# Optimization experiments

Hardware: AMD Instinct MI355X
Metric: run time of the kernel (lower is better)

The kernel has to match this reference:

```python
import jax, jax.numpy as jnp
import numpy as np

D_MODEL = 512
N_HEADS = 8
D_K = D_MODEL // N_HEADS


def setup_inputs() -> dict:
    key = jax.random.key(0)
    ks = jax.random.split(key, 7)
    s = 1.0 / np.sqrt(D_MODEL)
    return {
        "x": jax.random.normal(ks[0], (2, 4096, D_MODEL), dtype=jnp.float32),
        "W_q": jax.random.normal(ks[1], (D_MODEL, D_MODEL), dtype=jnp.float32) * s,
        "W_k": jax.random.normal(ks[2], (D_MODEL, D_MODEL), dtype=jnp.float32) * s,
        "W_v": jax.random.normal(ks[3], (D_MODEL, D_MODEL), dtype=jnp.float32) * s,
        "b_v": jax.random.normal(ks[4], (D_MODEL,), dtype=jnp.float32) * s,
        "W_o": jax.random.normal(ks[5], (D_MODEL, D_MODEL), dtype=jnp.float32) * s,
        "b_o": jax.random.normal(ks[6], (D_MODEL,), dtype=jnp.float32) * s,
    }


def _split_heads(t):
    # [N, S, d_model] -> [N, H, S, d_k]
    N, S, _ = t.shape
    return t.reshape(N, S, N_HEADS, D_K).transpose(0, 2, 1, 3)


def reference(x, W_q, W_k, W_v, b_v, W_o, b_o):
    N, S, _ = x.shape
    # nn.Linear computes x @ W.T (+ b)
    Q = _split_heads(x @ W_q.T)
    K = _split_heads(x @ W_k.T)
    V = _split_heads(x @ W_v.T + b_v)
    scale = jnp.sqrt(jnp.asarray(D_K, x.dtype))
    scores = jnp.einsum('nhqd,nhkd->nhqk', Q, K) / scale  # [N,H,S,S]
    causal = jnp.tril(jnp.ones((S, S), dtype=bool))
    scores = jnp.where(causal, scores, -jnp.inf)
    attn = jax.nn.softmax(scores, axis=-1)
    out = jnp.einsum('nhqk,nhkd->nhqd', attn, V)  # [N,H,S,d_k]
    out = out.transpose(0, 2, 1, 3).reshape(N, S, D_MODEL)
    return out @ W_o.T + b_o
```

## Files before the change

### kernel.cpp

```cpp
#include <hip/hip_runtime.h>
#include <hip/hip_bf16.h>

#define NB 2
#define SEQ 4096
#define DM 512
#define NH 8
#define DKH 64
#define MTOT (NB*SEQ)

typedef __attribute__((ext_vector_type(4))) float f32x4;
typedef __attribute__((ext_vector_type(16))) float f32x16;
typedef __attribute__((ext_vector_type(8))) short bf16x8;
typedef __attribute__((ext_vector_type(2))) unsigned uint2v;

__device__ inline unsigned short f2bf(float f) {
    union { float f; unsigned int u; } v; v.f = f;
    unsigned int r = v.u + 0x7FFFu + ((v.u >> 16) & 1u);
    return (unsigned short)(r >> 16);
}

#define QSCALE 0.18033688011112042f

__global__ void cast_kernel(const float* __restrict__ x, const float* __restrict__ wq,
                            const float* __restrict__ wk, const float* __restrict__ wv,
                            const float* __restrict__ wo, unsigned short* __restrict__ dst) {
    const int NX = MTOT*DM;
    const int NW = DM*DM;
    int i4 = blockIdx.x * blockDim.x + threadIdx.x;
    long e = (long)i4 * 4;
    if (e >= NX + 4L*NW) return;
    const float* src; long off;
    if (e < NX)           { src = x;  off = e; }
    else if (e < NX+NW)   { src = wq; off = e - NX; }
    else if (e < NX+2*NW) { src = wk; off = e - NX - NW; }
    else if (e < NX+3*NW) { src = wv; off = e - NX - 2*NW; }
    else                  { src = wo; off = e - NX - 3*NW; }
    float4 v = *reinterpret_cast<const float4*>(src + off);
    ushort4 o;
    o.x = f2bf(v.x); o.y = f2bf(v.y); o.z = f2bf(v.z); o.w = f2bf(v.w);
    *reinterpret_cast<ushort4*>(dst + e) = o;
}

template<int MODE>
__global__ __launch_bounds__(256, 2) void gemm_bt(
    const unsigned short* __restrict__ A,
    const unsigned short* __restrict__ B,
    const float* __restrict__ bias,
    unsigned short* __restrict__ Qh, unsigned short* __restrict__ Kh,
    unsigned short* __restrict__ Vt,
    float* __restrict__ Cout)
{
    const int K = 512;
    __shared__ __align__(16) unsigned short As[128*64];
    __shared__ __align__(16) unsigned short Bs[128*64];
    int tid = threadIdx.x;
    int wid = tid >> 6, lane = tid & 63;
    int wr = wid >> 1, wc = wid & 1;
    int brow = blockIdx.x * 128;
    int bcol = blockIdx.y * 128;
    int l15 = lane & 15, l4 = lane >> 4;

    f32x4 acc[4][4] = {};

    for (int kt = 0; kt < K/64; ++kt) {
        __syncthreads();
        #pragma unroll
        for (int i = 0; i < 4; ++i) {
            int rbase = i*32 + wid*8;
            int row = rbase + (lane >> 3);
            int csrc = (lane & 7) ^ (row & 7);
            const unsigned short* asrc = A + (long)(brow+row)*K + kt*64 + csrc*8;
            __builtin_amdgcn_global_load_lds(
                (const __attribute__((address_space(1))) unsigned int*)asrc,
                (__attribute__((address_space(3))) unsigned int*)&As[rbase*64], 16, 0, 0);
            const unsigned short* bsrc = B + (long)(bcol+row)*K + kt*64 + csrc*8;
            __builtin_amdgcn_global_load_lds(
                (const __attribute__((address_space(1))) unsigned int*)bsrc,
                (__attribute__((address_space(3))) unsigned int*)&Bs[rbase*64], 16, 0, 0);
        }
        __syncthreads();
        #pragma unroll
        for (int kk = 0; kk < 2; ++kk) {
            bf16x8 af[4], bfr[4];
            #pragma unroll
            for (int mi = 0; mi < 4; ++mi) {
                int row = wr*64 + mi*16 + l15;
                int colb = (kk*32 + l4*8) * 2;
                af[mi] = *reinterpret_cast<const bf16x8*>(
                    reinterpret_cast<const char*>(As) + row*128 + (colb ^ ((row&7)<<4)));
            }
            #pragma unroll
            for (int ni = 0; ni < 4; ++ni) {
                int row = wc*64 + ni*16 + l15;
                int colb = (kk*32 + l4*8) * 2;
                bfr[ni] = *reinterpret_cast<const bf16x8*>(
                    reinterpret_cast<const char*>(Bs) + row*128 + (colb ^ ((row&7)<<4)));
            }
            #pragma unroll
            for (int mi = 0; mi < 4; ++mi)
                #pragma unroll
                for (int ni = 0; ni < 4; ++ni)
                    acc[mi][ni] = __builtin_amdgcn_mfma_f32_16x16x32_bf16(af[mi], bfr[ni], acc[mi][ni], 0, 0, 0);
        }
    }

    #pragma unroll
    for (int mi = 0; mi < 4; ++mi) {
        #pragma unroll
        for (int ni = 0; ni < 4; ++ni) {
            #pragma unroll
            for (int r = 0; r < 4; ++r) {
                int row = brow + wr*64 + mi*16 + l4*4 + r;
                int col = bcol + wc*64 + ni*16 + l15;
                float v = acc[mi][ni][r];
                if (MODE == 0) {
                    int which = col >> 9;
                    int cw = col & 511;
                    int h = cw >> 6, d = cw & 63;
                    int b = row >> 12, s = row & 4095;
                    int bh = b*NH + h;
                    if (which == 0) {
                        Qh[((long)(bh*SEQ + s))*DKH + d] = f2bf(v * QSCALE);
                    } else if (which == 1) {
                        Kh[((long)(bh*SEQ + s))*DKH + d] = f2bf(v);
                    } else {
                        Vt[((long)(bh*DKH + d))*SEQ + s] = f2bf(v + bias[cw]);
                    }
                } else {
                    Cout[(long)row*DM + col] = v + bias[col];
                }
            }
        }
    }
}

__global__ __launch_bounds__(256, 2) void attn_kernel(
    const unsigned short* __restrict__ Qh,
    const unsigned short* __restrict__ Kh,
    const unsigned short* __restrict__ Vt,
    unsigned short* __restrict__ Obf)
{
    __shared__ __align__(16) unsigned short Klds[2][8448];
    __shared__ __align__(16) unsigned short Vlds[2][8448];
    const int tid = threadIdx.x;
    const int wid = tid >> 6, lane = tid & 63;
    const int l31 = lane & 31;
    const int hi  = lane >> 5;
    const int bh  = blockIdx.x;
    const int ty  = blockIdx.y;
    const int tile = ty < 16 ? 31 - ty : ty - 16;

    const unsigned short* Qbase = Qh + (long)bh*SEQ*DKH;
    const unsigned short* Kbase = Kh + (long)bh*SEQ*DKH;
    const unsigned short* Vbase = Vt + (long)bh*DKH*SEQ;

    const int q0w = tile*128 + wid*32;
    const int q   = q0w + l31;
    const int nt  = tile + 1;
    const int swz   = (l31 & 7) << 4;
    const int lbase = (l31 >> 3)*1056 + (l31 & 7)*128;

    bf16x8 qf[4];
    #pragma unroll
    for (int kk = 0; kk < 4; ++kk)
        qf[kk] = *reinterpret_cast<const bf16x8*>(Qbase + (long)q*DKH + kk*16 + hi*8);

    auto STAGE = [&](int b, int key0) {
        #pragma unroll
        for (int ii = 0; ii < 4; ++ii) {
            const int row = wid*32 + ii*8 + (lane >> 3);
            const int ck = (lane & 7) ^ (row & 7);
            const unsigned short* ksrc = Kbase + (long)(key0 + row)*DKH + ck*8;
            __builtin_amdgcn_global_load_lds(
                (const __attribute__((address_space(1))) unsigned int*)ksrc,
                (__attribute__((address_space(3))) unsigned int*)&Klds[b][(wid*4 + ii)*528], 16, 0, 0);
        }
        #pragma unroll
        for (int jj = 0; jj < 2; ++jj) {
            #pragma unroll
            for (int ii = 0; ii < 2; ++ii) {
                const int row = wid*16 + ii*8 + (lane >> 3);
                const int ck = (lane & 7) ^ (row & 7);
                const unsigned short* vsrc = Vbase + (long)row*SEQ + key0 + jj*64 + ck*8;
                __builtin_amdgcn_global_load_lds(
                    (const __attribute__((address_space(1))) unsigned int*)vsrc,
                    (__attribute__((address_space(3))) unsigned int*)&Vlds[b][(jj*8 + wid*2 + ii)*528], 16, 0, 0);
            }
        }
    };

    float m = -1e30f, lsum = 0.f;
    f32x16 od0 = {}, od1 = {};

    STAGE(0, 0);
    __syncthreads();
    int cur = 0;

    for (int kb = 0; kb < nt; ++kb) {
        if (kb + 1 < nt) STAGE(cur ^ 1, (kb + 1) << 7);
        const char* kl = reinterpret_cast<const char*>(Klds[cur]);
        const char* vl = reinterpret_cast<const char*>(Vlds[cur]);
        const int key0 = kb << 7;

        bf16x8 kfr[4][4];
        #pragma unroll
        for (int kk = 0; kk < 4; ++kk) {
            const int co = (kk*32 + hi*16) ^ swz;
            #pragma unroll
            for (int c = 0; c < 4; ++c)
                kfr[kk][c] = *reinterpret_cast<const bf16x8*>(kl + lbase + c*4224 + co);
        }
        f32x16 s0 = {}, s1 = {}, s2 = {}, s3 = {};
        __builtin_amdgcn_s_setprio(1);
        #pragma unroll
        for (int kk = 0; kk < 4; ++kk) {
            s0 = __builtin_amdgcn_mfma_f32_32x32x16_bf16(kfr[kk][0], qf[kk], s0, 0, 0, 0);
            s1 = __builtin_amdgcn_mfma_f32_32x32x16_bf16(kfr[kk][1], qf[kk], s1, 0, 0, 0);
            s2 = __builtin_amdgcn_mfma_f32_32x32x16_bf16(kfr[kk][2], qf[kk], s2, 0, 0, 0);
            s3 = __builtin_amdgcn_mfma_f32_32x32x16_bf16(kfr[kk][3], qf[kk], s3, 0, 0, 0);
        }
        __builtin_amdgcn_s_setprio(0);

        if (key0 + 127 > q0w) {
            #pragma unroll
            for (int r = 0; r < 16; ++r) {
                const int ko = (r&3) + 8*(r>>2) + 4*hi;
                if (key0 + ko > q)      s0[r] = -1e30f;
                if (key0 + 32 + ko > q) s1[r] = -1e30f;
                if (key0 + 64 + ko > q) s2[r] = -1e30f;
                if (key0 + 96 + ko > q) s3[r] = -1e30f;
            }
        }

        float pmax = s0[0];
        #pragma unroll
        for (int r = 1; r < 16; ++r) pmax = fmaxf(pmax, s0[r]);
        #pragma unroll
        for (int r = 0; r < 16; ++r) pmax = fmaxf(pmax, fmaxf(s1[r], fmaxf(s2[r], s3[r])));
        {
            uint2v pr = __builtin_amdgcn_permlane32_swap(__float_as_uint(pmax), __float_as_uint(pmax), false, false);
            pmax = fmaxf(__uint_as_float(pr[0]), __uint_as_float(pr[1]));
        }

        if (__any(pmax > m + 6.0f)) {
            const float mn = fmaxf(m, pmax);
            const float alpha = __builtin_amdgcn_exp2f(m - mn);
            m = mn;
            lsum *= alpha;
            #pragma unroll
            for (int r = 0; r < 16; ++r) { od0[r] *= alpha; od1[r] *= alpha; }
        }

        float rsc0 = 0.f, rsc1 = 0.f, rsc2 = 0.f, rsc3 = 0.f;
#define EXP_CHUNK(SV, RS) do {                                                     \
        _Pragma("unroll")                                                          \
        for (int r = 0; r < 16; ++r) {                                             \
            SV[r] = __builtin_amdgcn_exp2f(SV[r] - m);                             \
            RS += SV[r];                                                           \
        } } while (0)

#define PV_STEP(SV, VBASE, KS, B0) do {                                            \
        unsigned c0, c1, c2, c3;                                                   \
        float t0 = SV[B0+0], t1 = SV[B0+1], t2 = SV[B0+2], t3 = SV[B0+3];          \
        float t4 = SV[B0+4], t5 = SV[B0+5], t6 = SV[B0+6], t7 = SV[B0+7];          \
        asm("v_cvt_pk_bf16_f32 %0, %1, %2" : "=v"(c0) : "v"(t0), "v"(t1));         \
        asm("v_cvt_pk_bf16_f32 %0, %1, %2" : "=v"(c1) : "v"(t2), "v"(t3));         \
        asm("v_cvt_pk_bf16_f32 %0, %1, %2" : "=v"(c2) : "v"(t4), "v"(t5));         \
        asm("v_cvt_pk_bf16_f32 %0, %1, %2" : "=v"(c3) : "v"(t6), "v"(t7));         \
        uint2v sw0 = __builtin_amdgcn_permlane32_swap(c0, c2, false, false);       \
        uint2v sw1 = __builtin_amdgcn_permlane32_swap(c1, c3, false, false);       \
        union { unsigned u[4]; bf16x8 v; } pu;                                     \
        pu.u[0] = sw0[0]; pu.u[1] = sw1[0]; pu.u[2] = sw0[1]; pu.u[3] = sw1[1];    \
        bf16x8 vf0 = *reinterpret_cast<const bf16x8*>(VBASE + lbase +        (((KS)*32 + hi*16) ^ swz)); \
        od0 = __builtin_amdgcn_mfma_f32_32x32x16_bf16(vf0, pu.v, od0, 0, 0, 0);    \
        bf16x8 vf1 = *reinterpret_cast<const bf16x8*>(VBASE + lbase + 4224 + (((KS)*32 + hi*16) ^ swz)); \
        od1 = __builtin_amdgcn_mfma_f32_32x32x16_bf16(vf1, pu.v, od1, 0, 0, 0);    \
    } while (0)

        const char* vl0 = vl;
        const char* vl1 = vl + 8448;
        EXP_CHUNK(s0, rsc0);
        PV_STEP(s0, vl0, 0, 0);
        PV_STEP(s0, vl0, 1, 8);
        EXP_CHUNK(s1, rsc1);
        PV_STEP(s1, vl0, 2, 0);
        PV_STEP(s1, vl0, 3, 8);
        EXP_CHUNK(s2, rsc2);
        PV_STEP(s2, vl1, 0, 0);
        PV_STEP(s2, vl1, 1, 8);
        EXP_CHUNK(s3, rsc3);
        PV_STEP(s3, vl1, 2, 0);
        PV_STEP(s3, vl1, 3, 8);
#undef PV_STEP
#undef EXP_CHUNK
        lsum += (rsc0 + rsc1) + (rsc2 + rsc3);

        __syncthreads();
        cur ^= 1;
    }

    {
        uint2v pr = __builtin_amdgcn_permlane32_swap(__float_as_uint(lsum), __float_as_uint(lsum), false, false);
        lsum = __uint_as_float(pr[0]) + __uint_as_float(pr[1]);
    }
    const float rls = 1.0f / lsum;
    const long obase = (long)((bh >> 3)*SEQ + q)*DM + (bh & 7)*DKH;
    #pragma unroll
    for (int rr = 0; rr < 4; ++rr) {
        ushort4 w0, w1;
        w0.x = f2bf(od0[rr*4+0]*rls); w0.y = f2bf(od0[rr*4+1]*rls);
        w0.z = f2bf(od0[rr*4+2]*rls); w0.w = f2bf(od0[rr*4+3]*rls);
        *reinterpret_cast<ushort4*>(Obf + obase + rr*8 + hi*4) = w0;
        w1.x = f2bf(od1[rr*4+0]*rls); w1.y = f2bf(od1[rr*4+1]*rls);
        w1.z = f2bf(od1[rr*4+2]*rls); w1.w = f2bf(od1[rr*4+3]*rls);
        *reinterpret_cast<ushort4*>(Obf + obase + 32 + rr*8 + hi*4) = w1;
    }
}

extern "C" void kernel_launch(void* const* d_in, const int* in_sizes, int n_in,
                              void* d_out, int out_size, void* d_ws, size_t ws_size,
                              hipStream_t stream) {
    const float* x  = (const float*)d_in[0];
    const float* wq = (const float*)d_in[1];
    const float* wk = (const float*)d_in[2];
    const float* wv = (const float*)d_in[3];
    const float* bv = (const float*)d_in[4];
    const float* wo = (const float*)d_in[5];
    const float* bo = (const float*)d_in[6];
    float* out = (float*)d_out;

    unsigned short* ws = (unsigned short*)d_ws;
    unsigned short* Xbf  = ws;
    unsigned short* Wqkv = Xbf  + 4194304;
    unsigned short* Wob  = Wqkv + 786432;
    unsigned short* Qh   = Wob  + 262144;
    unsigned short* Kh   = Qh   + 4194304;
    unsigned short* Vt   = Kh   + 4194304;
    unsigned short* Obf  = Vt   + 4194304;

    cast_kernel<<<5120, 256, 0, stream>>>(x, wq, wk, wv, wo, Xbf);

    dim3 g1(64, 12);
    gemm_bt<0><<<g1, 256, 0, stream>>>(Xbf, Wqkv, bv, Qh, Kh, Vt, nullptr);

    dim3 g2(16, 32);
    attn_kernel<<<g2, 256, 0, stream>>>(Qh, Kh, Vt, Obf);

    dim3 g3(64, 4);
    gemm_bt<1><<<g3, 256, 0, stream>>>(Obf, Wob, bo, nullptr, nullptr, nullptr, out);
}
```

Measured before the change: 121.3 us.

## Pair complementary 64-query causal tiles per 2-wave attention block

The attention kernel drops from 4 waves per block to 2 waves of 128 threads. Each block now processes two 64-query tiles in sequence, tile 63-ty and tile ty, so every block does about the same causal work. The LDS K/V buffers lose their padded row stride and rely only on the XOR swizzle, and launch bounds allow more registers per thread. In exchange, each staged 128-key K/V tile now serves only 64 queries, which doubles K/V load traffic. Each CU also holds fewer resident waves, and diagonal 128-key blocks waste some masked work for 64-query tiles.

```diff
diff --git a/kernel.cpp b/kernel.cpp
--- a/kernel.cpp
+++ b/kernel.cpp
@@ -134,186 +134,194 @@
     }
 }
 
-__global__ __launch_bounds__(256, 2) void attn_kernel(
+__global__ __launch_bounds__(128, 1) void attn_kernel(
     const unsigned short* __restrict__ Qh,
     const unsigned short* __restrict__ Kh,
     const unsigned short* __restrict__ Vt,
     unsigned short* __restrict__ Obf)
 {
-    __shared__ __align__(16) unsigned short Klds[2][8448];
-    __shared__ __align__(16) unsigned short Vlds[2][8448];
+    __shared__ __align__(16) unsigned short Klds[2][128*64];
+    __shared__ __align__(16) unsigned short Vlds[2][2*64*64];
     const int tid = threadIdx.x;
     const int wid = tid >> 6, lane = tid & 63;
     const int l31 = lane & 31;
     const int hi  = lane >> 5;
     const int bh  = blockIdx.x;
     const int ty  = blockIdx.y;
-    const int tile = ty < 16 ? 31 - ty : ty - 16;
 
     const unsigned short* Qbase = Qh + (long)bh*SEQ*DKH;
     const unsigned short* Kbase = Kh + (long)bh*SEQ*DKH;
     const unsigned short* Vbase = Vt + (long)bh*DKH*SEQ;
 
-    const int q0w = tile*128 + wid*32;
-    const int q   = q0w + l31;
-    const int nt  = tile + 1;
-    const int swz   = (l31 & 7) << 4;
-    const int lbase = (l31 >> 3)*1056 + (l31 & 7)*128;
-
-    bf16x8 qf[4];
-    #pragma unroll
-    for (int kk = 0; kk < 4; ++kk)
-        qf[kk] = *reinterpret_cast<const bf16x8*>(Qbase + (long)q*DKH + kk*16 + hi*8);
-
-    auto STAGE = [&](int b, int key0) {
-        #pragma unroll
-        for (int ii = 0; ii < 4; ++ii) {
-            const int row = wid*32 + ii*8 + (lane >> 3);
+    const int swz = (l31 & 7) << 4;
+
+    auto STAGE_K = [&](int b, int key0) {
+        #pragma unroll
+        for (int ii = 0; ii < 8; ++ii) {
+            const int rbase = wid*64 + ii*8;
+            const int row = rbase + (lane >> 3);
             const int ck = (lane & 7) ^ (row & 7);
             const unsigned short* ksrc = Kbase + (long)(key0 + row)*DKH + ck*8;
             __builtin_amdgcn_global_load_lds(
                 (const __attribute__((address_space(1))) unsigned int*)ksrc,
-                (__attribute__((address_space(3))) unsigned int*)&Klds[b][(wid*4 + ii)*528], 16, 0, 0);
-        }
+                (__attribute__((address_space(3))) unsigned int*)&Klds[b][rbase*64], 16, 0, 0);
+        }
+    };
+    auto STAGE_V = [&](int b, int key0) {
         #pragma unroll
         for (int jj = 0; jj < 2; ++jj) {
             #pragma unroll
-            for (int ii = 0; ii < 2; ++ii) {
-                const int row = wid*16 + ii*8 + (lane >> 3);
+            for (int ii = 0; ii < 4; ++ii) {
+                const int rbase = wid*32 + ii*8;
+                const int row = rbase + (lane >> 3);
                 const int ck = (lane & 7) ^ (row & 7);
                 const unsigned short* vsrc = Vbase + (long)row*SEQ + key0 + jj*64 + ck*8;
                 __builtin_amdgcn_global_load_lds(
                     (const __attribute__((address_space(1))) unsigned int*)vsrc,
-                    (__attribute__((address_space(3))) unsigned int*)&Vlds[b][(jj*8 + wid*2 + ii)*528], 16, 0, 0);
+                    (__attribute__((address_space(3))) unsigned int*)&Vlds[b][jj*4096 + rbase*64], 16, 0, 0);
             }
         }
     };
 
-    float m = -1e30f, lsum = 0.f;
-    f32x16 od0 = {}, od1 = {};
-
-    STAGE(0, 0);
-    __syncthreads();
-    int cur = 0;
-
-    for (int kb = 0; kb < nt; ++kb) {
-        if (kb + 1 < nt) STAGE(cur ^ 1, (kb + 1) << 7);
-        const char* kl = reinterpret_cast<const char*>(Klds[cur]);
-        const char* vl = reinterpret_cast<const char*>(Vlds[cur]);
-        const int key0 = kb << 7;
-
-        bf16x8 kfr[4][4];
-        #pragma unroll
-        for (int kk = 0; kk < 4; ++kk) {
-            const int co = (kk*32 + hi*16) ^ swz;
-            #pragma unroll
-            for (int c = 0; c < 4; ++c)
-                kfr[kk][c] = *reinterpret_cast<const bf16x8*>(kl + lbase + c*4224 + co);
-        }
-        f32x16 s0 = {}, s1 = {}, s2 = {}, s3 = {};
-        __builtin_amdgcn_s_setprio(1);
-        #pragma unroll
-        for (int kk = 0; kk < 4; ++kk) {
-            s0 = __builtin_amdgcn_mfma_f32_32x32x16_bf16(kfr[kk][0], qf[kk], s0, 0, 0, 0);
-            s1 = __builtin_amdgcn_mfma_f32_32x32x16_bf16(kfr[kk][1], qf[kk], s1, 0, 0, 0);
-            s2 = __builtin_amdgcn_mfma_f32_32x32x16_bf16(kfr[kk][2], qf[kk], s2, 0, 0, 0);
-            s3 = __builtin_amdgcn_mfma_f32_32x32x16_bf16(kfr[kk][3], qf[kk], s3, 0, 0, 0);
-        }
-        __builtin_amdgcn_s_setprio(0);
-
-        if (key0 + 127 > q0w) {
-            #pragma unroll
-            for (int r = 0; r < 16; ++r) {
-                const int ko = (r&3) + 8*(r>>2) + 4*hi;
-                if (key0 + ko > q)      s0[r] = -1e30f;
-                if (key0 + 32 + ko > q) s1[r] = -1e30f;
-                if (key0 + 64 + ko > q) s2[r] = -1e30f;
-                if (key0 + 96 + ko > q) s3[r] = -1e30f;
-            }
-        }
-
-        float pmax = s0[0];
-        #pragma unroll
-        for (int r = 1; r < 16; ++r) pmax = fmaxf(pmax, s0[r]);
-        #pragma unroll
-        for (int r = 0; r < 16; ++r) pmax = fmaxf(pmax, fmaxf(s1[r], fmaxf(s2[r], s3[r])));
-        {
-            uint2v pr = __builtin_amdgcn_permlane32_swap(__float_as_uint(pmax), __float_as_uint(pmax), false, false);
-            pmax = fmaxf(__uint_as_float(pr[0]), __uint_as_float(pr[1]));
-        }
-
-        if (__any(pmax > m + 6.0f)) {
-            const float mn = fmaxf(m, pmax);
-            const float alpha = __builtin_amdgcn_exp2f(m - mn);
-            m = mn;
-            lsum *= alpha;
-            #pragma unroll
-            for (int r = 0; r < 16; ++r) { od0[r] *= alpha; od1[r] *= alpha; }
-        }
-
-        float rsc0 = 0.f, rsc1 = 0.f, rsc2 = 0.f, rsc3 = 0.f;
+    #pragma unroll 1
+    for (int half = 0; half < 2; ++half) {
+        const int tile = half ? ty : 63 - ty;
+        const int q0w = tile*64 + wid*32;
+        const int q   = q0w + l31;
+        const int nt  = (tile >> 1) + 1;
+
+        bf16x8 qf[4];
+        #pragma unroll
+        for (int kk = 0; kk < 4; ++kk)
+            qf[kk] = *reinterpret_cast<const bf16x8*>(Qbase + (long)q*DKH + kk*16 + hi*8);
+
+        float m = -1e30f, lsum = 0.f;
+        f32x16 od0 = {}, od1 = {};
+
+        STAGE_K(0, 0);
+        STAGE_V(0, 0);
+        __syncthreads();
+        int cur = 0;
+
+        for (int kb = 0; kb < nt; ++kb) {
+            if (kb + 1 < nt) { STAGE_K(cur ^ 1, (kb + 1) << 7); STAGE_V(cur ^ 1, (kb + 1) << 7); }
+            const char* kl = reinterpret_cast<const char*>(Klds[cur]);
+            const char* vl = reinterpret_cast<const char*>(Vlds[cur]);
+            const int key0 = kb << 7;
+
+            bf16x8 kfr[4][4];
+            #pragma unroll
+            for (int kk = 0; kk < 4; ++kk) {
+                const int co = (kk*32 + hi*16) ^ swz;
+                #pragma unroll
+                for (int c = 0; c < 4; ++c)
+                    kfr[kk][c] = *reinterpret_cast<const bf16x8*>(kl + (c*32 + l31)*128 + co);
+            }
+            f32x16 s0 = {}, s1 = {}, s2 = {}, s3 = {};
+            __builtin_amdgcn_s_setprio(1);
+            #pragma unroll
+            for (int kk = 0; kk < 4; ++kk) {
+                s0 = __builtin_amdgcn_mfma_f32_32x32x16_bf16(kfr[kk][0], qf[kk], s0, 0, 0, 0);
+                s1 = __builtin_amdgcn_mfma_f32_32x32x16_bf16(kfr[kk][1], qf[kk], s1, 0, 0, 0);
+                s2 = __builtin_amdgcn_mfma_f32_32x32x16_bf16(kfr[kk][2], qf[kk], s2, 0, 0, 0);
+                s3 = __builtin_amdgcn_mfma_f32_32x32x16_bf16(kfr[kk][3], qf[kk], s3, 0, 0, 0);
+            }
+            __builtin_amdgcn_s_setprio(0);
+
+            if (key0 + 127 > q0w) {
+                #pragma unroll
+                for (int r = 0; r < 16; ++r) {
+                    const int ko = (r&3) + 8*(r>>2) + 4*hi;
+                    if (key0 + ko > q)      s0[r] = -1e30f;
+                    if (key0 + 32 + ko > q) s1[r] = -1e30f;
+                    if (key0 + 64 + ko > q) s2[r] = -1e30f;
+                    if (key0 + 96 + ko > q) s3[r] = -1e30f;
+                }
+            }
+
+            float pmax = s0[0];
+            #pragma unroll
+            for (int r = 1; r < 16; ++r) pmax = fmaxf(pmax, s0[r]);
+            #pragma unroll
+            for (int r = 0; r < 16; ++r) pmax = fmaxf(pmax, fmaxf(s1[r], fmaxf(s2[r], s3[r])));
+            {
+                uint2v pr = __builtin_amdgcn_permlane32_swap(__float_as_uint(pmax), __float_as_uint(pmax), false, false);
+                pmax = fmaxf(__uint_as_float(pr[0]), __uint_as_float(pr[1]));
+            }
+
+            if (__any(pmax > m + 6.0f)) {
+                const float mn = fmaxf(m, pmax);
+                const float alpha = __builtin_amdgcn_exp2f(m - mn);
+                m = mn;
+                lsum *= alpha;
+                #pragma unroll
+                for (int r = 0; r < 16; ++r) { od0[r] *= alpha; od1[r] *= alpha; }
+            }
+
+            float rsc0 = 0.f, rsc1 = 0.f, rsc2 = 0.f, rsc3 = 0.f;
 #define EXP_CHUNK(SV, RS) do {                                                     \
-        _Pragma("unroll")                                                          \
-        for (int r = 0; r < 16; ++r) {                                             \
-            SV[r] = __builtin_amdgcn_exp2f(SV[r] - m);                             \
-            RS += SV[r];                                                           \
-        } } while (0)
-
-#define PV_STEP(SV, VBASE, KS, B0) do {                                            \
-        unsigned c0, c1, c2, c3;                                                   \
-        float t0 = SV[B0+0], t1 = SV[B0+1], t2 = SV[B0+2], t3 = SV[B0+3];          \
-        float t4 = SV[B0+4], t5 = SV[B0+5], t6 = SV[B0+6], t7 = SV[B0+7];          \
-        asm("v_cvt_pk_bf16_f32 %0, %1, %2" : "=v"(c0) : "v"(t0), "v"(t1));         \
-        asm("v_cvt_pk_bf16_f32 %0, %1, %2" : "=v"(c1) : "v"(t2), "v"(t3));         \
-        asm("v_cvt_pk_bf16_f32 %0, %1, %2" : "=v"(c2) : "v"(t4), "v"(t5));         \
-        asm("v_cvt_pk_bf16_f32 %0, %1, %2" : "=v"(c3) : "v"(t6), "v"(t7));         \
-        uint2v sw0 = __builtin_amdgcn_permlane32_swap(c0, c2, false, false);       \
-        uint2v sw1 = __builtin_amdgcn_permlane32_swap(c1, c3, false, false);       \
-        union { unsigned u[4]; bf16x8 v; } pu;                                     \
-        pu.u[0] = sw0[0]; pu.u[1] = sw1[0]; pu.u[2] = sw0[1]; pu.u[3] = sw1[1];    \
-        bf16x8 vf0 = *reinterpret_cast<const bf16x8*>(VBASE + lbase +        (((KS)*32 + hi*16) ^ swz)); \
-        od0 = __builtin_amdgcn_mfma_f32_32x32x16_bf16(vf0, pu.v, od0, 0, 0, 0);    \
-        bf16x8 vf1 = *reinterpret_cast<const bf16x8*>(VBASE + lbase + 4224 + (((KS)*32 + hi*16) ^ swz)); \
-        od1 = __builtin_amdgcn_mfma_f32_32x32x16_bf16(vf1, pu.v, od1, 0, 0, 0);    \
-    } while (0)
-
-        const char* vl0 = vl;
-        const char* vl1 = vl + 8448;
-        EXP_CHUNK(s0, rsc0);
-        PV_STEP(s0, vl0, 0, 0);
-        PV_STEP(s0, vl0, 1, 8);
-        EXP_CHUNK(s1, rsc1);
-        PV_STEP(s1, vl0, 2, 0);
-        PV_STEP(s1, vl0, 3, 8);
-        EXP_CHUNK(s2, rsc2);
-        PV_STEP(s2, vl1, 0, 0);
-        PV_STEP(s2, vl1, 1, 8);
-        EXP_CHUNK(s3, rsc3);
-        PV_STEP(s3, vl1, 2, 0);
-        PV_STEP(s3, vl1, 3, 8);
+            _Pragma("unroll")                                                      \
+            for (int r = 0; r < 16; ++r) {                                         \
+                SV[r] = __builtin_amdgcn_exp2f(SV[r] - m);                         \
+                RS += SV[r];                                                       \
+            } } while (0)
+
+#define PV_STEP(SV, VLS, KS, B0) do {                                              \
+            unsigned c0, c1, c2, c3;                                               \
+            float t0 = SV[B0+0], t1 = SV[B0+1], t2 = SV[B0+2], t3 = SV[B0+3];      \
+            float t4 = SV[B0+4], t5 = SV[B0+5], t6 = SV[B0+6], t7 = SV[B0+7];      \
+            asm("v_cvt_pk_bf16_f32 %0, %1, %2" : "=v"(c0) : "v"(t0), "v"(t1));     \
+            asm("v_cvt_pk_bf16_f32 %0, %1, %2" : "=v"(c1) : "v"(t2), "v"(t3));     \
+            asm("v_cvt_pk_bf16_f32 %0, %1, %2" : "=v"(c2) : "v"(t4), "v"(t5));     \
+            asm("v_cvt_pk_bf16_f32 %0, %1, %2" : "=v"(c3) : "v"(t6), "v"(t7));     \
+            uint2v sw0 = __builtin_amdgcn_permlane32_swap(c0, c2, false, false);   \
+            uint2v sw1 = __builtin_amdgcn_permlane32_swap(c1, c3, false, false);   \
+            union { unsigned u[4]; bf16x8 v; } pu;                                 \
+            pu.u[0] = sw0[0]; pu.u[1] = sw1[0]; pu.u[2] = sw0[1]; pu.u[3] = sw1[1];\
+            bf16x8 vf0 = *reinterpret_cast<const bf16x8*>(VLS + l31*128      + (((KS)*32 + hi*16) ^ swz)); \
+            od0 = __builtin_amdgcn_mfma_f32_32x32x16_bf16(vf0, pu.v, od0, 0, 0, 0);\
+            bf16x8 vf1 = *reinterpret_cast<const bf16x8*>(VLS + (32+l31)*128 + (((KS)*32 + hi*16) ^ swz)); \
+            od1 = __builtin_amdgcn_mfma_f32_32x32x16_bf16(vf1, pu.v, od1, 0, 0, 0);\
+        } while (0)
+
+            const char* vl0 = vl;
+            const char* vl1 = vl + 8192;
+            EXP_CHUNK(s0, rsc0);
+            PV_STEP(s0, vl0, 0, 0);
+            PV_STEP(s0, vl0, 1, 8);
+            EXP_CHUNK(s1, rsc1);
+            PV_STEP(s1, vl0, 2, 0);
+            PV_STEP(s1, vl0, 3, 8);
+            EXP_CHUNK(s2, rsc2);
+            PV_STEP(s2, vl1, 0, 0);
+            PV_STEP(s2, vl1, 1, 8);
+            EXP_CHUNK(s3, rsc3);
+            PV_STEP(s3, vl1, 2, 0);
+            PV_STEP(s3, vl1, 3, 8);
 #undef PV_STEP
 #undef EXP_CHUNK
-        lsum += (rsc0 + rsc1) + (rsc2 + rsc3);
-
-        __syncthreads();
-        cur ^= 1;
-    }
-
-    {
-        uint2v pr = __builtin_amdgcn_permlane32_swap(__float_as_uint(lsum), __float_as_uint(lsum), false, false);
-        lsum = __uint_as_float(pr[0]) + __uint_as_float(pr[1]);
-    }
-    const float rls = 1.0f / lsum;
-    const long obase = (long)((bh >> 3)*SEQ + q)*DM + (bh & 7)*DKH;
-    #pragma unroll
-    for (int rr = 0; rr < 4; ++rr) {
-        ushort4 w0, w1;
-        w0.x = f2bf(od0[rr*4+0]*rls); w0.y = f2bf(od0[rr*4+1]*rls);
-        w0.z = f2bf(od0[rr*4+2]*rls); w0.w = f2bf(od0[rr*4+3]*rls);
-        *reinterpret_cast<ushort4*>(Obf + obase + rr*8 + hi*4) = w0;
-        w1.x = f2bf(od1[rr*4+0]*rls); w1.y = f2bf(od1[rr*4+1]*rls);
-        w1.z = f2bf(od1[rr*4+2]*rls); w1.w = f2bf(od1[rr*4+3]*rls);
-        *reinterpret_cast<ushort4*>(Obf + obase + 32 + rr*8 + hi*4) = w1;
+            lsum += (rsc0 + rsc1) + (rsc2 + rsc3);
+
+            __syncthreads();
+            cur ^= 1;
+        }
+
+        {
+            uint2v pr = __builtin_amdgcn_permlane32_swap(__float_as_uint(lsum), __float_as_uint(lsum), false, false);
+            lsum = __uint_as_float(pr[0]) + __uint_as_float(pr[1]);
+        }
+        const float rls = 1.0f / lsum;
+        const long obase = (long)((bh >> 3)*SEQ + q)*DM + (bh & 7)*DKH;
+        #pragma unroll
+        for (int rr = 0; rr < 4; ++rr) {
+            ushort4 w0, w1;
+            w0.x = f2bf(od0[rr*4+0]*rls); w0.y = f2bf(od0[rr*4+1]*rls);
+            w0.z = f2bf(od0[rr*4+2]*rls); w0.w = f2bf(od0[rr*4+3]*rls);
+            *reinterpret_cast<ushort4*>(Obf + obase + rr*8 + hi*4) = w0;
+            w1.x = f2bf(od1[rr*4+0]*rls); w1.y = f2bf(od1[rr*4+1]*rls);
+            w1.z = f2bf(od1[rr*4+2]*rls); w1.w = f2bf(od1[rr*4+3]*rls);
+            *reinterpret_cast<ushort4*>(Obf + obase + 32 + rr*8 + hi*4) = w1;
+        }
     }
 }
 
@@ -344,7 +352,7 @@
     gemm_bt<0><<<g1, 256, 0, stream>>>(Xbf, Wqkv, bv, Qh, Kh, Vt, nullptr);
 
     dim3 g2(16, 32);
-    attn_kernel<<<g2, 256, 0, stream>>>(Qh, Kh, Vt, Obf);
+    attn_kernel<<<g2, 128, 0, stream>>>(Qh, Kh, Vt, Obf);
 
     dim3 g3(64, 4);
     gemm_bt<1><<<g3, 256, 0, stream>>>(Obf, Wob, bo, nullptr, nullptr, nullptr, out);
```

Result: slower. 128.4 us (+5.9%).
